# Optimization experiments

Hardware: AMD Instinct MI355X
Metric: run time of the kernel (lower is better)

The kernel has to match this reference:

```python
import jax, jax.numpy as jnp
import numpy as np

NQ = 4      # n_qubits
T = 512     # seq_lenght
H = 1024    # hidden_size
F = 64      # input feature size
B = 16      # batch size (hardcoded in original module)


def _circuit_tables(nq):
    idx = np.arange(2 ** nq)
    # BasicEntanglerLayers CNOT ring: (0,1),(1,2),...,(n-1,0) for n>2; single CNOT for n==2
    pairs = [(i, (i + 1) % nq) for i in range(nq)] if nq > 2 else [(0, 1)]
    perms = []
    for c, t in pairs:  # CNOT as a basis-state permutation (qubit 0 = MSB)
        ctrl = (idx >> (nq - 1 - c)) & 1
        perms.append(idx ^ (ctrl << (nq - 1 - t)))
    bits = (idx[:, None] >> (nq - 1 - np.arange(nq))[None, :]) & 1
    signs = (1.0 - 2.0 * bits).astype(np.float32)  # (2**nq, nq), <Z_q> signs
    return perms, signs

_PERMS, _SIGNS = _circuit_tables(NQ)
_SIGNS_J = jnp.asarray(_SIGNS)


def circuit_expvals(theta):
    """theta: (..., NQ) total RX angle per wire (AngleEmbedding RX + entangler RX).
    Returns (..., NQ) PauliZ expvals after product-RX state + CNOT ring."""
    half = 0.5 * theta
    a0 = jnp.cos(half).astype(jnp.complex64)
    a1 = (-1j * jnp.sin(half)).astype(jnp.complex64)
    state = jnp.ones(theta.shape[:-1] + (1,), dtype=jnp.complex64)
    for q in range(NQ):  # build product state, qubit 0 most significant
        amp = jnp.stack([a0[..., q], a1[..., q]], axis=-1)
        state = (state[..., :, None] * amp[..., None, :]).reshape(theta.shape[:-1] + (-1,))
    for perm in _PERMS:  # CNOT ring = permutations of the computational basis
        state = state[..., perm]
    probs = state.real ** 2 + state.imag ** 2  # (..., 2**NQ)
    return probs @ _SIGNS_J                     # (..., NQ)


def qlstm_last(x, w4, Wy, by, Wf, bf, Wi, bi, Wu, bu, Wo, bo):
    """x: (B, T, feat). Dense params are stacked per-timestep along axis 0 (T,...)
    (the original creates a fresh nn.Dense every loop iteration).
    Returns the hidden state at the last timestep, (B, H)."""
    h0 = jnp.zeros((x.shape[0], H), dtype=x.dtype)
    c0 = jnp.zeros((x.shape[0], H), dtype=x.dtype)

    def step(carry, inp):
        h, c = carry
        x_t, wy, byt, wf, bft, wi, bit_, wu, but, wo, bot = inp
        v = jnp.concatenate([h, x_t], axis=1)
        y = v @ wy + byt                                   # (B, NQ)
        z = circuit_expvals(y[None] + w4[:, None, :])      # (4, B, NQ), shared input, 4 gate weights
        f = jax.nn.sigmoid(z[0]) @ wf + bft                # NOTE: no activation after Dense, as in source
        i = jax.nn.sigmoid(z[1]) @ wi + bit_
        g = jnp.tanh(z[2]) @ wu + but
        o = jax.nn.sigmoid(z[3]) @ wo + bot
        c = f * c + i * g
        h = o * jnp.tanh(c)
        return (h, c), None

    xs = (jnp.swapaxes(x, 0, 1), Wy, by, Wf, bf, Wi, bi, Wu, bu, Wo, bo)
    (h, _), _ = jax.lax.scan(step, (h0, c0), xs)
    return h


def setup_inputs() -> dict:
    key = jax.random.key(0)
    ks = jax.random.split(key, 16)
    def w(k, shape, fan_in):
        return jax.random.normal(k, shape, jnp.float32) / np.sqrt(fan_in)
    inp = {"x": jax.random.normal(ks[0], (B, T, F), jnp.float32)}
    # quantum weights (n_qlayers=1, n_qubits) per gate
    for n, k in zip(["qwf", "qwi", "qwu", "qwo"], jax.random.split(ks[1], 4)):
        inp[n] = jax.random.uniform(k, (1, NQ), jnp.float32, -1.0, 1.0)
    # encoder: per-timestep Dense stacks
    inp["Wy_e"] = w(ks[2], (T, H + F, NQ), H + F); inp["by_e"] = jnp.zeros((T, NQ), jnp.float32)
    for n, k in zip(["f", "i", "u", "o"], jax.random.split(ks[3], 4)):
        inp["W" + n + "_e"] = w(k, (T, NQ, H), NQ)
        inp["b" + n + "_e"] = jnp.zeros((T, H), jnp.float32)
    # decoder: input feature size 1
    inp["Wy_d"] = w(ks[4], (T, H + 1, NQ), H + 1); inp["by_d"] = jnp.zeros((T, NQ), jnp.float32)
    for n, k in zip(["f", "i", "u", "o"], jax.random.split(ks[5], 4)):
        inp["W" + n + "_d"] = w(k, (T, NQ, H), NQ)
        inp["b" + n + "_d"] = jnp.zeros((T, H), jnp.float32)
    # final Dense(seq_lenght)
    inp["Wt"] = w(ks[6], (H, T), H); inp["bt"] = jnp.zeros((T,), jnp.float32)
    return inp


def reference(x, qwf, qwi, qwu, qwo,
              Wy_e, by_e, Wf_e, bf_e, Wi_e, bi_e, Wu_e, bu_e, Wo_e, bo_e,
              Wy_d, by_d, Wf_d, bf_d, Wi_d, bi_d, Wu_d, bu_d, Wo_d, bo_d,
              Wt, bt):
    w4 = jnp.stack([qwf[0], qwi[0], qwu[0], qwo[0]])  # only layer-0 row is used by the qnode
    h_enc = qlstm_last(x, w4, Wy_e, by_e, Wf_e, bf_e, Wi_e, bi_e, Wu_e, bu_e, Wo_e, bo_e)
    x2 = h_enc[:, :, None]                 # (B, H, 1)
    h_dec = qlstm_last(x2[:, :T, :], w4, Wy_d, by_d, Wf_d, bf_d, Wi_d, bi_d, Wu_d, bu_d, Wo_d, bo_d)
    target = h_dec @ Wt + bt               # (B, T)
    return target[:, :, None]              # (B, T, 1)
```

## Files before the change

kernel.cpp:

```cpp
#include <hip/hip_runtime.h>

#define Tn 512
#define Hn 1024
#define Fn 64
#define NTH 512
#define NW (NTH / 64)

#define STEPB (6u * 512u * 16u)
#define MAXTOFF (511u * STEPB)
#define REC_PASS ((unsigned long long)Tn * STEPB)
#define YXE_OFF (2ull * REC_PASS)
#define WS_NEED (2ull * REC_PASS + 16ull * 512ull * 16ull)

typedef unsigned u32x4 __attribute__((ext_vector_type(4)));
typedef __fp16 h2 __attribute__((ext_vector_type(2)));

struct QParams {
  const float *x;
  const float *qw0, *qw1, *qw2, *qw3;
  const float *Wy_e, *by_e, *Wf_e, *bf_e, *Wi_e, *bi_e, *Wu_e, *bu_e, *Wo_e, *bo_e;
  const float *Wy_d, *by_d, *Wf_d, *bf_d, *Wi_d, *bi_d, *Wu_d, *bu_d, *Wo_d, *bo_d;
  const float *Wt, *bt;
  float *out;
};

#define BAR()                                                                  \
  do {                                                                         \
    asm volatile("s_waitcnt lgkmcnt(0)" ::: "memory");                         \
    __builtin_amdgcn_s_barrier();                                              \
    asm volatile("" ::: "memory");                                             \
  } while (0)
#define WAIT_VM(N)                                                             \
  do {                                                                         \
    asm volatile("s_waitcnt vmcnt(" #N ")" ::: "memory");                      \
    __builtin_amdgcn_sched_barrier(0);                                         \
  } while (0)

template <int CTRL, int RM, int BM, bool BC>
__device__ __forceinline__ float dppadd(float x) {
  int t = __builtin_amdgcn_update_dpp(0, __builtin_bit_cast(int, x), CTRL, RM,
                                      BM, BC);
  return x + __builtin_bit_cast(float, t);
}
template <int CTRL>
__device__ __forceinline__ float dppmov(float x) {
  int t = __builtin_amdgcn_update_dpp(0, __builtin_bit_cast(int, x), CTRL, 0xF,
                                      0xF, true);
  return __builtin_bit_cast(float, t);
}
__device__ __forceinline__ float wave_sum63(float x) {
  x = dppadd<0xB1, 0xF, 0xF, true>(x);
  x = dppadd<0x4E, 0xF, 0xF, true>(x);
  x = dppadd<0x141, 0xF, 0xF, true>(x);
  x = dppadd<0x140, 0xF, 0xF, true>(x);
  x = dppadd<0x142, 0xA, 0xF, false>(x);
  x = dppadd<0x143, 0xC, 0xF, false>(x);
  return x;
}
__device__ __forceinline__ float tanhc(float c) {
  float e = __builtin_amdgcn_exp2f(c * 2.885390081777927f);
  return fmaf(-2.f, __builtin_amdgcn_rcpf(e + 1.f), 1.f);
}
__device__ __forceinline__ h2 pk2(float a, float b) {
  return __builtin_amdgcn_cvt_pkrtz(a, b);
}
__device__ __forceinline__ h2 uh(unsigned u) { return __builtin_bit_cast(h2, u); }
__device__ __forceinline__ float fdot2f(h2 a, h2 b, float c) {
#if __has_builtin(__builtin_amdgcn_fdot2)
  return __builtin_amdgcn_fdot2(a, b, c, false);
#else
  float d;
  asm("v_dot2_f32_f16 %0, %1, %2, %3" : "=v"(d) : "v"(a), "v"(b), "v"(c));
  return d;
#endif
}
__device__ __forceinline__ unsigned pkh(float a, float b) {
  h2 h;
  h.x = (__fp16)a;
  h.y = (__fp16)b;
  return __builtin_bit_cast(unsigned, h);
}

struct LaneCtx {
  int tid, lane, wid;
  unsigned jt16;
  bool q1, q2;
  float w4lane;
  float mlane, alane, klane;
};
struct SBase {
  unsigned long long a[6];
};

__global__ __launch_bounds__(512) void qprep_kernel(QParams p, char *ws) {
  int t = blockIdx.x;
  const bool dec = (t >= 512);
  if (dec) t -= 512;
  const int j = threadIdx.x;

  const float *Wg0 = dec ? p.Wf_d : p.Wf_e, *Wg1 = dec ? p.Wi_d : p.Wi_e;
  const float *Wg2 = dec ? p.Wu_d : p.Wu_e, *Wg3 = dec ? p.Wo_d : p.Wo_e;
  const float *bf = dec ? p.bf_d : p.bf_e, *bi = dec ? p.bi_d : p.bi_e;
  const float *bu = dec ? p.bu_d : p.bu_e, *bo = dec ? p.bo_d : p.bo_e;
  const float *Wy = dec ? p.Wy_d : p.Wy_e;
  const int K = dec ? (Hn + 1) : (Hn + Fn);

  u32x4 *dst = (u32x4 *)(ws + (dec ? REC_PASS : 0));
  const int rbase = t * 6 * 512 + j;
  const int t4 = t * 4096;
  const float *Wg[4] = {Wg0, Wg1, Wg2, Wg3};
#pragma unroll
  for (int g = 0; g < 4; ++g) {
    u32x4 v;
    v.x = pkh(Wg[g][t4 + 0 * 1024 + j], Wg[g][t4 + 1 * 1024 + j]);
    v.y = pkh(Wg[g][t4 + 2 * 1024 + j], Wg[g][t4 + 3 * 1024 + j]);
    v.z = pkh(Wg[g][t4 + 0 * 1024 + j + 512], Wg[g][t4 + 1 * 1024 + j + 512]);
    v.w = pkh(Wg[g][t4 + 2 * 1024 + j + 512], Wg[g][t4 + 3 * 1024 + j + 512]);
    dst[rbase + g * 512] = v;
  }
  {
    const int tb = t * 1024;
    u32x4 v = {pkh(bf[tb + j], bf[tb + j + 512]),
               pkh(bi[tb + j], bi[tb + j + 512]),
               pkh(bu[tb + j], bu[tb + j + 512]),
               pkh(bo[tb + j], bo[tb + j + 512])};
    dst[rbase + 4 * 512] = v;
  }
  {
    const float4 w0 = *(const float4 *)(Wy + ((size_t)t * K + j) * 4);
    const float4 w1 = *(const float4 *)(Wy + ((size_t)t * K + j + 512) * 4);
    u32x4 v = {pkh(w0.x, w1.x), pkh(w0.y, w1.y), pkh(w0.z, w1.z),
               pkh(w0.w, w1.w)};
    dst[rbase + 5 * 512] = v;
  }

  if (!dec && j < 16) {
    const int b = j;
    float a0 = p.by_e[t * 4 + 0], a1 = p.by_e[t * 4 + 1],
          a2 = p.by_e[t * 4 + 2], a3 = p.by_e[t * 4 + 3];
#pragma unroll 8
    for (int k = 0; k < 64; ++k) {
      const float xv = p.x[((size_t)b * Tn + t) * Fn + k];
      const float4 wr =
          *(const float4 *)(p.Wy_e + ((size_t)t * (Hn + Fn) + Hn + k) * 4);
      a0 = fmaf(xv, wr.x, a0);
      a1 = fmaf(xv, wr.y, a1);
      a2 = fmaf(xv, wr.z, a2);
      a3 = fmaf(xv, wr.w, a3);
    }
    ((float4 *)(ws + YXE_OFF))[(size_t)b * Tn + t] =
        make_float4(a0, a1, a2, a3);
  }
}

struct Regs {
  u32x4 c0, c1, c2, c3, c4, c5;
};

__device__ __forceinline__ void issue_pf(Regs &r, const SBase &sb,
                                         unsigned voff) {
  asm volatile("global_load_dwordx4 %0, %1, %2" : "=v"(r.c5) : "v"(voff), "s"(sb.a[5]));
  asm volatile("global_load_dwordx4 %0, %1, %2" : "=v"(r.c0) : "v"(voff), "s"(sb.a[0]));
  asm volatile("global_load_dwordx4 %0, %1, %2" : "=v"(r.c1) : "v"(voff), "s"(sb.a[1]));
  asm volatile("global_load_dwordx4 %0, %1, %2" : "=v"(r.c2) : "v"(voff), "s"(sb.a[2]));
  asm volatile("global_load_dwordx4 %0, %1, %2" : "=v"(r.c3) : "v"(voff), "s"(sb.a[3]));
  asm volatile("global_load_dwordx4 %0, %1, %2" : "=v"(r.c4) : "v"(voff), "s"(sb.a[4]));
}

template <int PAR>
__device__ __forceinline__ void
qstep(int t, Regs &r, unsigned &toff, const SBase &sb, const LaneCtx &L,
      float *red_t, const float *yxby_l, float &h0, float &h1, float &c0,
      float &c1, h2 &hp) {
  const float yxs = yxby_l[t * 4 + (L.lane & 3)];
  WAIT_VM(18);
  float a0 = fdot2f(hp, uh(r.c5.x), 0.f);
  float a1 = fdot2f(hp, uh(r.c5.y), 0.f);
  float a2 = fdot2f(hp, uh(r.c5.z), 0.f);
  float a3 = fdot2f(hp, uh(r.c5.w), 0.f);
  a0 = wave_sum63(a0);
  a1 = wave_sum63(a1);
  a2 = wave_sum63(a2);
  a3 = wave_sum63(a3);
  if (L.lane == 63) {
    red_t[PAR * 32 + 0 * 8 + L.wid] = a0;
    red_t[PAR * 32 + 1 * 8 + L.wid] = a1;
    red_t[PAR * 32 + 2 * 8 + L.wid] = a2;
    red_t[PAR * 32 + 3 * 8 + L.wid] = a3;
  }
  BAR();
  const float4 rA = *(const float4 *)&red_t[PAR * 32 + (L.lane & 3) * 8 + 0];
  const float4 rB = *(const float4 *)&red_t[PAR * 32 + (L.lane & 3) * 8 + 4];
  const float yq =
      ((rA.x + rA.y) + (rA.z + rA.w)) + ((rB.x + rB.y) + (rB.z + rB.w));
  const float ang = yq + yxs + L.w4lane;
  const float cc = __cosf(ang);
  const float t1 = dppmov<0xB1>(cc);
  const float d1 = cc * t1;
  const float t2 = dppmov<0x4E>(d1);
  const float d2 = d1 * t2;
  const float zu = t1 * t2;
  const float zv = cc * t2;
  const float z = L.q2 ? (L.q1 ? d2 : zv) : (L.q1 ? d1 : zu);
  const float s =
      __builtin_amdgcn_rcpf(1.f + __builtin_amdgcn_exp2f(L.klane * z));
  const float act = fmaf(s, L.mlane, L.alane);
  const float actn = dppmov<0xB1>(act);
  const unsigned apk = __builtin_bit_cast(unsigned, pk2(act, actn));
  const h2 F01 = uh((unsigned)__builtin_amdgcn_readlane(apk, 0));
  const h2 F23 = uh((unsigned)__builtin_amdgcn_readlane(apk, 2));
  const h2 I01 = uh((unsigned)__builtin_amdgcn_readlane(apk, 4));
  const h2 I23 = uh((unsigned)__builtin_amdgcn_readlane(apk, 6));
  const h2 U01 = uh((unsigned)__builtin_amdgcn_readlane(apk, 8));
  const h2 U23 = uh((unsigned)__builtin_amdgcn_readlane(apk, 10));
  const h2 O01 = uh((unsigned)__builtin_amdgcn_readlane(apk, 12));
  const h2 O23 = uh((unsigned)__builtin_amdgcn_readlane(apk, 14));
  const h2 bgf = uh(r.c4.x), bgi = uh(r.c4.y), bgu = uh(r.c4.z),
           bgo = uh(r.c4.w);
  const float fv0 = fdot2f(F01, uh(r.c0.x), fdot2f(F23, uh(r.c0.y), (float)bgf.x));
  const float fv1 = fdot2f(F01, uh(r.c0.z), fdot2f(F23, uh(r.c0.w), (float)bgf.y));
  const float iv0 = fdot2f(I01, uh(r.c1.x), fdot2f(I23, uh(r.c1.y), (float)bgi.x));
  const float iv1 = fdot2f(I01, uh(r.c1.z), fdot2f(I23, uh(r.c1.w), (float)bgi.y));
  const float uv0 = fdot2f(U01, uh(r.c2.x), fdot2f(U23, uh(r.c2.y), (float)bgu.x));
  const float uv1 = fdot2f(U01, uh(r.c2.z), fdot2f(U23, uh(r.c2.w), (float)bgu.y));
  const float ov0 = fdot2f(O01, uh(r.c3.x), fdot2f(O23, uh(r.c3.y), (float)bgo.x));
  const float ov1 = fdot2f(O01, uh(r.c3.z), fdot2f(O23, uh(r.c3.w), (float)bgo.y));
  c0 = fmaf(fv0, c0, iv0 * uv0);
  h0 = ov0 * tanhc(c0);
  c1 = fmaf(fv1, c1, iv1 * uv1);
  h1 = ov1 * tanhc(c1);
  hp = pk2(h0, h1);
  issue_pf(r, sb, L.jt16 + toff);
  toff = toff + STEPB;
  if (toff > MAXTOFF) toff = MAXTOFF;
}

__device__ __forceinline__ void run_pass(const SBase &sb, const LaneCtx &L,
                                         float *red_t, const float *yxby_l,
                                         float &h0, float &h1, float &c0,
                                         float &c1) {
  Regs R0, R1, R2, R3;
  issue_pf(R0, sb, L.jt16 + 0 * STEPB);
  issue_pf(R1, sb, L.jt16 + 1 * STEPB);
  issue_pf(R2, sb, L.jt16 + 2 * STEPB);
  issue_pf(R3, sb, L.jt16 + 3 * STEPB);
  unsigned toff = 4 * STEPB;
  h2 hp = pk2(0.f, 0.f);
  for (int t = 0; t < Tn; t += 4) {
    qstep<0>(t + 0, R0, toff, sb, L, red_t, yxby_l, h0, h1, c0, c1, hp);
    qstep<1>(t + 1, R1, toff, sb, L, red_t, yxby_l, h0, h1, c0, c1, hp);
    qstep<0>(t + 2, R2, toff, sb, L, red_t, yxby_l, h0, h1, c0, c1, hp);
    qstep<1>(t + 3, R3, toff, sb, L, red_t, yxby_l, h0, h1, c0, c1, hp);
  }
  asm volatile("s_waitcnt vmcnt(0)" ::: "memory");
  __builtin_amdgcn_sched_barrier(0);
}

__global__ __launch_bounds__(NTH, 2) void qlstm_f16_kernel(QParams p,
                                                           char *ws) {
  const int b = blockIdx.x;
  LaneCtx L;
  L.tid = threadIdx.x;
  L.lane = L.tid & 63;
  L.wid = L.tid >> 6;
  L.jt16 = (unsigned)L.tid * 16u;
  const int q = L.lane & 3, g = (L.lane >> 2) & 3;
  L.q1 = q & 1;
  L.q2 = q & 2;
  {
    const float *qwp =
        (g == 0) ? p.qw0 : (g == 1) ? p.qw1 : (g == 2) ? p.qw2 : p.qw3;
    L.w4lane = qwp[q];
  }
  L.mlane = (g == 2) ? 2.f : 1.f;
  L.alane = 1.f - L.mlane;
  L.klane = -L.mlane * 1.4426950408889634f;

  __shared__ __align__(16) float red_t[2 * 4 * 8];
  __shared__ __align__(16) float yxby_l[Tn * 4];
  __shared__ __align__(16) float hbuf[Hn];

  SBase sbE, sbD;
#pragma unroll
  for (int k = 0; k < 6; ++k) {
    sbE.a[k] = (unsigned long long)ws + (unsigned long long)k * 8192ull;
    sbD.a[k] = (unsigned long long)ws + REC_PASS + (unsigned long long)k * 8192ull;
  }

  ((float4 *)yxby_l)[L.tid] =
      ((const float4 *)(ws + YXE_OFF))[(size_t)b * Tn + L.tid];
  float h0 = 0.f, h1 = 0.f, c0 = 0.f, c1 = 0.f;
  __syncthreads();

  run_pass(sbE, L, red_t, yxby_l, h0, h1, c0, c1);

  __syncthreads();
  hbuf[L.tid] = h0;
  hbuf[L.tid + NTH] = h1;
  __syncthreads();
  {
    const float hv = hbuf[L.tid];
    const float4 wx =
        *(const float4 *)(p.Wy_d + ((size_t)L.tid * (Hn + 1) + Hn) * 4);
    const float4 bd = *(const float4 *)(p.by_d + L.tid * 4);
    ((float4 *)yxby_l)[L.tid] =
        make_float4(fmaf(hv, wx.x, bd.x), fmaf(hv, wx.y, bd.y),
                    fmaf(hv, wx.z, bd.z), fmaf(hv, wx.w, bd.w));
  }
  h0 = h1 = c0 = c1 = 0.f;
  __syncthreads();

  run_pass(sbD, L, red_t, yxby_l, h0, h1, c0, c1);

  __syncthreads();
  hbuf[L.tid] = h0;
  hbuf[L.tid + NTH] = h1;
  __syncthreads();
  {
    float acc = p.bt[L.tid];
    const float4 *h4 = (const float4 *)hbuf;
#pragma unroll 4
    for (int j4 = 0; j4 < Hn / 4; ++j4) {
      const float4 hv = h4[j4];
      acc = fmaf(hv.x, p.Wt[(j4 * 4 + 0) * Tn + L.tid], acc);
      acc = fmaf(hv.y, p.Wt[(j4 * 4 + 1) * Tn + L.tid], acc);
      acc = fmaf(hv.z, p.Wt[(j4 * 4 + 2) * Tn + L.tid], acc);
      acc = fmaf(hv.w, p.Wt[(j4 * 4 + 3) * Tn + L.tid], acc);
    }
    p.out[(size_t)b * Tn + L.tid] = acc;
  }
}

__device__ __forceinline__ float sum8_all(float x) {
  x = dppadd<0xB1, 0xF, 0xF, true>(x);
  x = dppadd<0x4E, 0xF, 0xF, true>(x);
  x = dppadd<0x141, 0xF, 0xF, true>(x);
  return x;
}

struct WB {
  float w[32];
  float bb[8];
  float4 wy0, wy1;
  float4 wyx;
  float xv;
};

template <bool DEC>
__device__ __forceinline__ WB
pf_fb(int t, int b, int tid, const float *__restrict__ x,
      const float *__restrict__ Wy, const float *__restrict__ Wf,
      const float *__restrict__ bfp, const float *__restrict__ Wi,
      const float *__restrict__ bip, const float *__restrict__ Wu,
      const float *__restrict__ bup, const float *__restrict__ Wo,
      const float *__restrict__ bop) {
  WB d;
  const int K = DEC ? (Hn + 1) : (Hn + Fn);
  const int g0 = t * 4096 + tid;
#pragma unroll
  for (int e = 0; e < 2; ++e) {
    const int ge = g0 + e * 512;
#pragma unroll
    for (int n = 0; n < 4; ++n) {
      d.w[e * 16 + 0 * 4 + n] = Wf[ge + n * 1024];
      d.w[e * 16 + 1 * 4 + n] = Wi[ge + n * 1024];
      d.w[e * 16 + 2 * 4 + n] = Wu[ge + n * 1024];
      d.w[e * 16 + 3 * 4 + n] = Wo[ge + n * 1024];
    }
    const int be = t * 1024 + tid + e * 512;
    d.bb[e * 4 + 0] = bfp[be];
    d.bb[e * 4 + 1] = bip[be];
    d.bb[e * 4 + 2] = bup[be];
    d.bb[e * 4 + 3] = bop[be];
  }
  d.wy0 = *(const float4 *)(Wy + (t * K + tid) * 4);
  d.wy1 = *(const float4 *)(Wy + (t * K + tid + 512) * 4);
  if (!DEC) {
    if (tid < Fn) {
      d.wyx = *(const float4 *)(Wy + (t * K + Hn + tid) * 4);
      d.xv = x[(b * Tn + t) * Fn + tid];
    }
  } else {
    if (tid == 0) d.wyx = *(const float4 *)(Wy + (t * K + Hn) * 4);
  }
  return d;
}

template <bool DEC, int PAR>
__device__ __forceinline__ void
step_fb(int t, int tn, const WB &rd, WB &wr, int b, const LaneCtx &L,
        const float *__restrict__ x, const float *__restrict__ Wy,
        const float *__restrict__ Wf, const float *__restrict__ bfp,
        const float *__restrict__ Wi, const float *__restrict__ bip,
        const float *__restrict__ Wu, const float *__restrict__ bup,
        const float *__restrict__ Wo, const float *__restrict__ bop,
        float4 (*red4)[NW], const float *by_l, const float *henc_s, float &h0,
        float &h1, float &c0, float &c1) {
  float a0 = h0 * rd.wy0.x, a1 = h0 * rd.wy0.y, a2 = h0 * rd.wy0.z,
        a3 = h0 * rd.wy0.w;
  a0 = fmaf(h1, rd.wy1.x, a0);
  a1 = fmaf(h1, rd.wy1.y, a1);
  a2 = fmaf(h1, rd.wy1.z, a2);
  a3 = fmaf(h1, rd.wy1.w, a3);
  if (!DEC) {
    if (L.tid < Fn) {
      a0 = fmaf(rd.xv, rd.wyx.x, a0);
      a1 = fmaf(rd.xv, rd.wyx.y, a1);
      a2 = fmaf(rd.xv, rd.wyx.z, a2);
      a3 = fmaf(rd.xv, rd.wyx.w, a3);
    }
  } else {
    if (L.tid == 0) {
      const float xv = henc_s[t];
      a0 = fmaf(xv, rd.wyx.x, a0);
      a1 = fmaf(xv, rd.wyx.y, a1);
      a2 = fmaf(xv, rd.wyx.z, a2);
      a3 = fmaf(xv, rd.wyx.w, a3);
    }
  }
  a0 = wave_sum63(a0);
  a1 = wave_sum63(a1);
  a2 = wave_sum63(a2);
  a3 = wave_sum63(a3);
  if (L.lane == 63) red4[PAR][L.wid] = make_float4(a0, a1, a2, a3);
  wr = pf_fb<DEC>(tn, b, L.tid, x, Wy, Wf, bfp, Wi, bip, Wu, bup, Wo, bop);
  BAR();
  float4 rv = red4[PAR][L.lane & 7];
  const float byq = by_l[t * 4 + (L.lane & 3)];
  float y0 = sum8_all(rv.x), y1 = sum8_all(rv.y), y2 = sum8_all(rv.z),
        y3 = sum8_all(rv.w);
  const float yq = L.q2 ? (L.q1 ? y3 : y2) : (L.q1 ? y1 : y0);
  const float ang = yq + byq + L.w4lane;
  const float cc = __cosf(ang);
  const float t1 = dppmov<0xB1>(cc);
  const float d1 = cc * t1;
  const float t2 = dppmov<0x4E>(d1);
  const float d2 = d1 * t2;
  const float zu = t1 * t2;
  const float zv = cc * t2;
  const float z = L.q2 ? (L.q1 ? d2 : zv) : (L.q1 ? d1 : zu);
  const float s =
      __builtin_amdgcn_rcpf(1.f + __builtin_amdgcn_exp2f(L.klane * z));
  const float act = fmaf(s, L.mlane, L.alane);
#define RL(n)                                                                  \
  __builtin_bit_cast(float,                                                    \
                     __builtin_amdgcn_readlane(__builtin_bit_cast(int, act), n))
  const float f0 = RL(0), f1 = RL(1), f2 = RL(2), f3 = RL(3);
  const float i0 = RL(4), i1 = RL(5), i2 = RL(6), i3 = RL(7);
  const float u0 = RL(8), u1 = RL(9), u2 = RL(10), u3 = RL(11);
  const float o0 = RL(12), o1 = RL(13), o2 = RL(14), o3 = RL(15);
#undef RL
#pragma unroll
  for (int e = 0; e < 2; ++e) {
    float fv = rd.bb[e * 4 + 0], iv = rd.bb[e * 4 + 1], uv = rd.bb[e * 4 + 2],
          ov = rd.bb[e * 4 + 3];
    fv = fmaf(f0, rd.w[e * 16 + 0], fv);
    fv = fmaf(f1, rd.w[e * 16 + 1], fv);
    fv = fmaf(f2, rd.w[e * 16 + 2], fv);
    fv = fmaf(f3, rd.w[e * 16 + 3], fv);
    iv = fmaf(i0, rd.w[e * 16 + 4], iv);
    iv = fmaf(i1, rd.w[e * 16 + 5], iv);
    iv = fmaf(i2, rd.w[e * 16 + 6], iv);
    iv = fmaf(i3, rd.w[e * 16 + 7], iv);
    uv = fmaf(u0, rd.w[e * 16 + 8], uv);
    uv = fmaf(u1, rd.w[e * 16 + 9], uv);
    uv = fmaf(u2, rd.w[e * 16 + 10], uv);
    uv = fmaf(u3, rd.w[e * 16 + 11], uv);
    ov = fmaf(o0, rd.w[e * 16 + 12], ov);
    ov = fmaf(o1, rd.w[e * 16 + 13], ov);
    ov = fmaf(o2, rd.w[e * 16 + 14], ov);
    ov = fmaf(o3, rd.w[e * 16 + 15], ov);
    float &cr = e ? c1 : c0;
    float &hr = e ? h1 : h0;
    const float cn = fmaf(fv, cr, iv * uv);
    cr = cn;
    hr = ov * tanhc(cn);
  }
}

template <bool DEC>
__device__ void lstm_pass_fb(int b, const LaneCtx &L,
                             const float *__restrict__ x,
                             const float *__restrict__ Wy,
                             const float *__restrict__ by,
                             const float *__restrict__ Wf,
                             const float *__restrict__ bfp,
                             const float *__restrict__ Wi,
                             const float *__restrict__ bip,
                             const float *__restrict__ Wu,
                             const float *__restrict__ bup,
                             const float *__restrict__ Wo,
                             const float *__restrict__ bop,
                             float4 (*red4)[NW], float *by_l,
                             const float *henc_s, float &h0, float &h1,
                             float &c0, float &c1) {
#pragma unroll
  for (int i = 0; i < (Tn * 4) / NTH; ++i)
    by_l[L.tid + i * NTH] = by[L.tid + i * NTH];
  __syncthreads();
  WB bufA = pf_fb<DEC>(0, b, L.tid, x, Wy, Wf, bfp, Wi, bip, Wu, bup, Wo, bop);
  WB bufB;
  for (int t = 0; t < Tn; t += 2) {
    step_fb<DEC, 0>(t, t + 1, bufA, bufB, b, L, x, Wy, Wf, bfp, Wi, bip, Wu,
                    bup, Wo, bop, red4, by_l, henc_s, h0, h1, c0, c1);
    step_fb<DEC, 1>(t + 1, (t + 2 < Tn) ? (t + 2) : (Tn - 1), bufB, bufA, b, L,
                    x, Wy, Wf, bfp, Wi, bip, Wu, bup, Wo, bop, red4, by_l,
                    henc_s, h0, h1, c0, c1);
  }
}

__global__ __launch_bounds__(NTH, 2) void qlstm_fb_kernel(QParams p) {
  const int b = blockIdx.x;
  LaneCtx L;
  L.tid = threadIdx.x;
  L.lane = L.tid & 63;
  L.wid = L.tid >> 6;
  L.jt16 = (unsigned)L.tid * 16u;
  const int q = L.lane & 3, g = (L.lane >> 2) & 3;
  L.q1 = q & 1;
  L.q2 = q & 2;
  {
    const float *qwp =
        (g == 0) ? p.qw0 : (g == 1) ? p.qw1 : (g == 2) ? p.qw2 : p.qw3;
    L.w4lane = qwp[q];
  }
  L.mlane = (g == 2) ? 2.f : 1.f;
  L.alane = 1.f - L.mlane;
  L.klane = -L.mlane * 1.4426950408889634f;

  __shared__ float4 red4[2][NW];
  __shared__ float by_l[Tn * 4];
  __shared__ float henc_s[Hn];
  __shared__ float hst[Hn];

  float h0 = 0.f, h1 = 0.f, c0 = 0.f, c1 = 0.f;

  lstm_pass_fb<false>(b, L, p.x, p.Wy_e, p.by_e, p.Wf_e, p.bf_e, p.Wi_e,
                      p.bi_e, p.Wu_e, p.bu_e, p.Wo_e, p.bo_e, red4, by_l,
                      henc_s, h0, h1, c0, c1);
  henc_s[L.tid] = h0;
  henc_s[L.tid + NTH] = h1;
  h0 = h1 = c0 = c1 = 0.f;
  __syncthreads();
  lstm_pass_fb<true>(b, L, nullptr, p.Wy_d, p.by_d, p.Wf_d, p.bf_d, p.Wi_d,
                     p.bi_d, p.Wu_d, p.bu_d, p.Wo_d, p.bo_d, red4, by_l,
                     henc_s, h0, h1, c0, c1);
  hst[L.tid] = h0;
  hst[L.tid + NTH] = h1;
  __syncthreads();
  {
    float acc = p.bt[L.tid];
    const float4 *h4 = (const float4 *)hst;
#pragma unroll 4
    for (int j4 = 0; j4 < Hn / 4; ++j4) {
      const float4 hv = h4[j4];
      acc = fmaf(hv.x, p.Wt[(j4 * 4 + 0) * Tn + L.tid], acc);
      acc = fmaf(hv.y, p.Wt[(j4 * 4 + 1) * Tn + L.tid], acc);
      acc = fmaf(hv.z, p.Wt[(j4 * 4 + 2) * Tn + L.tid], acc);
      acc = fmaf(hv.w, p.Wt[(j4 * 4 + 3) * Tn + L.tid], acc);
    }
    p.out[(size_t)b * Tn + L.tid] = acc;
  }
}

extern "C" void kernel_launch(void *const *d_in, const int *in_sizes, int n_in,
                              void *d_out, int out_size, void *d_ws,
                              size_t ws_size, hipStream_t stream) {
  QParams p;
  p.x = (const float *)d_in[0];
  p.qw0 = (const float *)d_in[1];
  p.qw1 = (const float *)d_in[2];
  p.qw2 = (const float *)d_in[3];
  p.qw3 = (const float *)d_in[4];
  p.Wy_e = (const float *)d_in[5];
  p.by_e = (const float *)d_in[6];
  p.Wf_e = (const float *)d_in[7];
  p.bf_e = (const float *)d_in[8];
  p.Wi_e = (const float *)d_in[9];
  p.bi_e = (const float *)d_in[10];
  p.Wu_e = (const float *)d_in[11];
  p.bu_e = (const float *)d_in[12];
  p.Wo_e = (const float *)d_in[13];
  p.bo_e = (const float *)d_in[14];
  p.Wy_d = (const float *)d_in[15];
  p.by_d = (const float *)d_in[16];
  p.Wf_d = (const float *)d_in[17];
  p.bf_d = (const float *)d_in[18];
  p.Wi_d = (const float *)d_in[19];
  p.bi_d = (const float *)d_in[20];
  p.Wu_d = (const float *)d_in[21];
  p.bu_d = (const float *)d_in[22];
  p.Wo_d = (const float *)d_in[23];
  p.bo_d = (const float *)d_in[24];
  p.Wt = (const float *)d_in[25];
  p.bt = (const float *)d_in[26];
  p.out = (float *)d_out;

  if (ws_size >= WS_NEED) {
    char *ws = (char *)d_ws;
    hipLaunchKernelGGL(qprep_kernel, dim3(1024), dim3(512), 0, stream, p, ws);
    hipLaunchKernelGGL(qlstm_f16_kernel, dim3(16), dim3(NTH), 0, stream, p,
                       ws);
  } else {
    hipLaunchKernelGGL(qlstm_fb_kernel, dim3(16), dim3(NTH), 0, stream, p);
  }
}
```

Measured before the change: 691.0 us.

## Halve recurrent-kernel block to 256 threads with four hidden units per thread

The fp16 recurrent kernel now runs 256 threads per batch block, and each thread owns four hidden units instead of two. The prep kernel repacks the weights into a 12-stream layout to match, and the per-step prefetch issues 12 loads. Fewer waves shrink the cross-wave reduction and barrier cost of each serial timestep. In exchange, each thread does twice the arithmetic, holds more registers for four in-flight prefetch buffers, and the memory latency per step is spread across fewer waves.

```diff
diff --git a/kernel.cpp b/kernel.cpp
--- a/kernel.cpp
+++ b/kernel.cpp
@@ -3,10 +3,10 @@
 #define Tn 512
 #define Hn 1024
 #define Fn 64
-#define NTH 512
+#define NTH 256
 #define NW (NTH / 64)
 
-#define STEPB (6u * 512u * 16u)
+#define STEPB (12u * 256u * 16u)
 #define MAXTOFF (511u * STEPB)
 #define REC_PASS ((unsigned long long)Tn * STEPB)
 #define YXE_OFF (2ull * REC_PASS)
@@ -89,10 +89,10 @@
   float mlane, alane, klane;
 };
 struct SBase {
-  unsigned long long a[6];
+  unsigned long long a[12];
 };
 
-__global__ __launch_bounds__(512) void qprep_kernel(QParams p, char *ws) {
+__global__ __launch_bounds__(256) void qprep_kernel(QParams p, char *ws) {
   int t = blockIdx.x;
   const bool dec = (t >= 512);
   if (dec) t -= 512;
@@ -105,33 +105,42 @@
   const float *Wy = dec ? p.Wy_d : p.Wy_e;
   const int K = dec ? (Hn + 1) : (Hn + Fn);
 
-  u32x4 *dst = (u32x4 *)(ws + (dec ? REC_PASS : 0));
-  const int rbase = t * 6 * 512 + j;
+  char *base = ws + (dec ? REC_PASS : 0) + (size_t)t * STEPB;
   const int t4 = t * 4096;
   const float *Wg[4] = {Wg0, Wg1, Wg2, Wg3};
 #pragma unroll
   for (int g = 0; g < 4; ++g) {
-    u32x4 v;
-    v.x = pkh(Wg[g][t4 + 0 * 1024 + j], Wg[g][t4 + 1 * 1024 + j]);
-    v.y = pkh(Wg[g][t4 + 2 * 1024 + j], Wg[g][t4 + 3 * 1024 + j]);
-    v.z = pkh(Wg[g][t4 + 0 * 1024 + j + 512], Wg[g][t4 + 1 * 1024 + j + 512]);
-    v.w = pkh(Wg[g][t4 + 2 * 1024 + j + 512], Wg[g][t4 + 3 * 1024 + j + 512]);
-    dst[rbase + g * 512] = v;
+#pragma unroll
+    for (int k = 0; k < 2; ++k) {
+      const int jb = j + 512 * k;
+      u32x4 v;
+      v.x = pkh(Wg[g][t4 + 0 * 1024 + jb], Wg[g][t4 + 1 * 1024 + jb]);
+      v.y = pkh(Wg[g][t4 + 2 * 1024 + jb], Wg[g][t4 + 3 * 1024 + jb]);
+      v.z = pkh(Wg[g][t4 + 0 * 1024 + jb + 256], Wg[g][t4 + 1 * 1024 + jb + 256]);
+      v.w = pkh(Wg[g][t4 + 2 * 1024 + jb + 256], Wg[g][t4 + 3 * 1024 + jb + 256]);
+      *(u32x4 *)(base + (g * 2 + k) * 4096 + j * 16) = v;
+    }
   }
   {
     const int tb = t * 1024;
-    u32x4 v = {pkh(bf[tb + j], bf[tb + j + 512]),
-               pkh(bi[tb + j], bi[tb + j + 512]),
-               pkh(bu[tb + j], bu[tb + j + 512]),
-               pkh(bo[tb + j], bo[tb + j + 512])};
-    dst[rbase + 4 * 512] = v;
+#pragma unroll
+    for (int k = 0; k < 2; ++k) {
+      const int jb = tb + j + 512 * k;
+      u32x4 v = {pkh(bf[jb], bf[jb + 256]), pkh(bi[jb], bi[jb + 256]),
+                 pkh(bu[jb], bu[jb + 256]), pkh(bo[jb], bo[jb + 256])};
+      *(u32x4 *)(base + (8 + k) * 4096 + j * 16) = v;
+    }
   }
   {
-    const float4 w0 = *(const float4 *)(Wy + ((size_t)t * K + j) * 4);
-    const float4 w1 = *(const float4 *)(Wy + ((size_t)t * K + j + 512) * 4);
-    u32x4 v = {pkh(w0.x, w1.x), pkh(w0.y, w1.y), pkh(w0.z, w1.z),
-               pkh(w0.w, w1.w)};
-    dst[rbase + 5 * 512] = v;
+#pragma unroll
+    for (int k = 0; k < 2; ++k) {
+      const int jb = j + 512 * k;
+      const float4 w0 = *(const float4 *)(Wy + ((size_t)t * K + jb) * 4);
+      const float4 w1 = *(const float4 *)(Wy + ((size_t)t * K + jb + 256) * 4);
+      u32x4 v = {pkh(w0.x, w1.x), pkh(w0.y, w1.y), pkh(w0.z, w1.z),
+                 pkh(w0.w, w1.w)};
+      *(u32x4 *)(base + (10 + k) * 4096 + j * 16) = v;
+    }
   }
 
   if (!dec && j < 16) {
@@ -154,45 +163,56 @@
 }
 
 struct Regs {
-  u32x4 c0, c1, c2, c3, c4, c5;
+  u32x4 g0, g1, g2, g3, g4, g5, g6, g7;
+  u32x4 b8, b9;
+  u32x4 w10, w11;
 };
 
 __device__ __forceinline__ void issue_pf(Regs &r, const SBase &sb,
                                          unsigned voff) {
-  asm volatile("global_load_dwordx4 %0, %1, %2" : "=v"(r.c5) : "v"(voff), "s"(sb.a[5]));
-  asm volatile("global_load_dwordx4 %0, %1, %2" : "=v"(r.c0) : "v"(voff), "s"(sb.a[0]));
-  asm volatile("global_load_dwordx4 %0, %1, %2" : "=v"(r.c1) : "v"(voff), "s"(sb.a[1]));
-  asm volatile("global_load_dwordx4 %0, %1, %2" : "=v"(r.c2) : "v"(voff), "s"(sb.a[2]));
-  asm volatile("global_load_dwordx4 %0, %1, %2" : "=v"(r.c3) : "v"(voff), "s"(sb.a[3]));
-  asm volatile("global_load_dwordx4 %0, %1, %2" : "=v"(r.c4) : "v"(voff), "s"(sb.a[4]));
+  asm volatile("global_load_dwordx4 %0, %1, %2" : "=v"(r.w10) : "v"(voff), "s"(sb.a[10]));
+  asm volatile("global_load_dwordx4 %0, %1, %2" : "=v"(r.w11) : "v"(voff), "s"(sb.a[11]));
+  asm volatile("global_load_dwordx4 %0, %1, %2" : "=v"(r.g0) : "v"(voff), "s"(sb.a[0]));
+  asm volatile("global_load_dwordx4 %0, %1, %2" : "=v"(r.g1) : "v"(voff), "s"(sb.a[1]));
+  asm volatile("global_load_dwordx4 %0, %1, %2" : "=v"(r.g2) : "v"(voff), "s"(sb.a[2]));
+  asm volatile("global_load_dwordx4 %0, %1, %2" : "=v"(r.g3) : "v"(voff), "s"(sb.a[3]));
+  asm volatile("global_load_dwordx4 %0, %1, %2" : "=v"(r.g4) : "v"(voff), "s"(sb.a[4]));
+  asm volatile("global_load_dwordx4 %0, %1, %2" : "=v"(r.g5) : "v"(voff), "s"(sb.a[5]));
+  asm volatile("global_load_dwordx4 %0, %1, %2" : "=v"(r.g6) : "v"(voff), "s"(sb.a[6]));
+  asm volatile("global_load_dwordx4 %0, %1, %2" : "=v"(r.g7) : "v"(voff), "s"(sb.a[7]));
+  asm volatile("global_load_dwordx4 %0, %1, %2" : "=v"(r.b8) : "v"(voff), "s"(sb.a[8]));
+  asm volatile("global_load_dwordx4 %0, %1, %2" : "=v"(r.b9) : "v"(voff), "s"(sb.a[9]));
 }
 
 template <int PAR>
 __device__ __forceinline__ void
 qstep(int t, Regs &r, unsigned &toff, const SBase &sb, const LaneCtx &L,
-      float *red_t, const float *yxby_l, float &h0, float &h1, float &c0,
-      float &c1, h2 &hp) {
+      float *red_t, const float *yxby_l, float &h0, float &h1, float &h2r,
+      float &h3, float &c0, float &c1, float &c2r, float &c3, h2 &hp0,
+      h2 &hp1) {
   const float yxs = yxby_l[t * 4 + (L.lane & 3)];
-  WAIT_VM(18);
-  float a0 = fdot2f(hp, uh(r.c5.x), 0.f);
-  float a1 = fdot2f(hp, uh(r.c5.y), 0.f);
-  float a2 = fdot2f(hp, uh(r.c5.z), 0.f);
-  float a3 = fdot2f(hp, uh(r.c5.w), 0.f);
+  WAIT_VM(36);
+  float a0 = fdot2f(hp0, uh(r.w10.x), 0.f);
+  float a1 = fdot2f(hp0, uh(r.w10.y), 0.f);
+  float a2 = fdot2f(hp0, uh(r.w10.z), 0.f);
+  float a3 = fdot2f(hp0, uh(r.w10.w), 0.f);
+  a0 = fdot2f(hp1, uh(r.w11.x), a0);
+  a1 = fdot2f(hp1, uh(r.w11.y), a1);
+  a2 = fdot2f(hp1, uh(r.w11.z), a2);
+  a3 = fdot2f(hp1, uh(r.w11.w), a3);
   a0 = wave_sum63(a0);
   a1 = wave_sum63(a1);
   a2 = wave_sum63(a2);
   a3 = wave_sum63(a3);
   if (L.lane == 63) {
-    red_t[PAR * 32 + 0 * 8 + L.wid] = a0;
-    red_t[PAR * 32 + 1 * 8 + L.wid] = a1;
-    red_t[PAR * 32 + 2 * 8 + L.wid] = a2;
-    red_t[PAR * 32 + 3 * 8 + L.wid] = a3;
+    red_t[PAR * 16 + 0 * 4 + L.wid] = a0;
+    red_t[PAR * 16 + 1 * 4 + L.wid] = a1;
+    red_t[PAR * 16 + 2 * 4 + L.wid] = a2;
+    red_t[PAR * 16 + 3 * 4 + L.wid] = a3;
   }
   BAR();
-  const float4 rA = *(const float4 *)&red_t[PAR * 32 + (L.lane & 3) * 8 + 0];
-  const float4 rB = *(const float4 *)&red_t[PAR * 32 + (L.lane & 3) * 8 + 4];
-  const float yq =
-      ((rA.x + rA.y) + (rA.z + rA.w)) + ((rB.x + rB.y) + (rB.z + rB.w));
+  const float4 rA = *(const float4 *)&red_t[PAR * 16 + (L.lane & 3) * 4];
+  const float yq = (rA.x + rA.y) + (rA.z + rA.w);
   const float ang = yq + yxs + L.w4lane;
   const float cc = __cosf(ang);
   const float t1 = dppmov<0xB1>(cc);
@@ -215,21 +235,36 @@
   const h2 U23 = uh((unsigned)__builtin_amdgcn_readlane(apk, 10));
   const h2 O01 = uh((unsigned)__builtin_amdgcn_readlane(apk, 12));
   const h2 O23 = uh((unsigned)__builtin_amdgcn_readlane(apk, 14));
-  const h2 bgf = uh(r.c4.x), bgi = uh(r.c4.y), bgu = uh(r.c4.z),
-           bgo = uh(r.c4.w);
-  const float fv0 = fdot2f(F01, uh(r.c0.x), fdot2f(F23, uh(r.c0.y), (float)bgf.x));
-  const float fv1 = fdot2f(F01, uh(r.c0.z), fdot2f(F23, uh(r.c0.w), (float)bgf.y));
-  const float iv0 = fdot2f(I01, uh(r.c1.x), fdot2f(I23, uh(r.c1.y), (float)bgi.x));
-  const float iv1 = fdot2f(I01, uh(r.c1.z), fdot2f(I23, uh(r.c1.w), (float)bgi.y));
-  const float uv0 = fdot2f(U01, uh(r.c2.x), fdot2f(U23, uh(r.c2.y), (float)bgu.x));
-  const float uv1 = fdot2f(U01, uh(r.c2.z), fdot2f(U23, uh(r.c2.w), (float)bgu.y));
-  const float ov0 = fdot2f(O01, uh(r.c3.x), fdot2f(O23, uh(r.c3.y), (float)bgo.x));
-  const float ov1 = fdot2f(O01, uh(r.c3.z), fdot2f(O23, uh(r.c3.w), (float)bgo.y));
+  const h2 bF01 = uh(r.b8.x), bI01 = uh(r.b8.y), bU01 = uh(r.b8.z),
+           bO01 = uh(r.b8.w);
+  const h2 bF23 = uh(r.b9.x), bI23 = uh(r.b9.y), bU23 = uh(r.b9.z),
+           bO23 = uh(r.b9.w);
+  const float fv0 = fdot2f(F01, uh(r.g0.x), fdot2f(F23, uh(r.g0.y), (float)bF01.x));
+  const float fv1 = fdot2f(F01, uh(r.g0.z), fdot2f(F23, uh(r.g0.w), (float)bF01.y));
+  const float fv2 = fdot2f(F01, uh(r.g1.x), fdot2f(F23, uh(r.g1.y), (float)bF23.x));
+  const float fv3 = fdot2f(F01, uh(r.g1.z), fdot2f(F23, uh(r.g1.w), (float)bF23.y));
+  const float iv0 = fdot2f(I01, uh(r.g2.x), fdot2f(I23, uh(r.g2.y), (float)bI01.x));
+  const float iv1 = fdot2f(I01, uh(r.g2.z), fdot2f(I23, uh(r.g2.w), (float)bI01.y));
+  const float iv2 = fdot2f(I01, uh(r.g3.x), fdot2f(I23, uh(r.g3.y), (float)bI23.x));
+  const float iv3 = fdot2f(I01, uh(r.g3.z), fdot2f(I23, uh(r.g3.w), (float)bI23.y));
+  const float uv0 = fdot2f(U01, uh(r.g4.x), fdot2f(U23, uh(r.g4.y), (float)bU01.x));
+  const float uv1 = fdot2f(U01, uh(r.g4.z), fdot2f(U23, uh(r.g4.w), (float)bU01.y));
+  const float uv2 = fdot2f(U01, uh(r.g5.x), fdot2f(U23, uh(r.g5.y), (float)bU23.x));
+  const float uv3 = fdot2f(U01, uh(r.g5.z), fdot2f(U23, uh(r.g5.w), (float)bU23.y));
+  const float ov0 = fdot2f(O01, uh(r.g6.x), fdot2f(O23, uh(r.g6.y), (float)bO01.x));
+  const float ov1 = fdot2f(O01, uh(r.g6.z), fdot2f(O23, uh(r.g6.w), (float)bO01.y));
+  const float ov2 = fdot2f(O01, uh(r.g7.x), fdot2f(O23, uh(r.g7.y), (float)bO23.x));
+  const float ov3 = fdot2f(O01, uh(r.g7.z), fdot2f(O23, uh(r.g7.w), (float)bO23.y));
   c0 = fmaf(fv0, c0, iv0 * uv0);
   h0 = ov0 * tanhc(c0);
   c1 = fmaf(fv1, c1, iv1 * uv1);
   h1 = ov1 * tanhc(c1);
-  hp = pk2(h0, h1);
+  c2r = fmaf(fv2, c2r, iv2 * uv2);
+  h2r = ov2 * tanhc(c2r);
+  c3 = fmaf(fv3, c3, iv3 * uv3);
+  h3 = ov3 * tanhc(c3);
+  hp0 = pk2(h0, h1);
+  hp1 = pk2(h2r, h3);
   issue_pf(r, sb, L.jt16 + toff);
   toff = toff + STEPB;
   if (toff > MAXTOFF) toff = MAXTOFF;
@@ -237,26 +272,28 @@
 
 __device__ __forceinline__ void run_pass(const SBase &sb, const LaneCtx &L,
                                          float *red_t, const float *yxby_l,
-                                         float &h0, float &h1, float &c0,
-                                         float &c1) {
+                                         float &h0, float &h1, float &h2r,
+                                         float &h3, float &c0, float &c1,
+                                         float &c2r, float &c3) {
   Regs R0, R1, R2, R3;
+  WAIT_VM(0);
   issue_pf(R0, sb, L.jt16 + 0 * STEPB);
   issue_pf(R1, sb, L.jt16 + 1 * STEPB);
   issue_pf(R2, sb, L.jt16 + 2 * STEPB);
   issue_pf(R3, sb, L.jt16 + 3 * STEPB);
   unsigned toff = 4 * STEPB;
-  h2 hp = pk2(0.f, 0.f);
+  h2 hp0 = pk2(0.f, 0.f), hp1 = pk2(0.f, 0.f);
   for (int t = 0; t < Tn; t += 4) {
-    qstep<0>(t + 0, R0, toff, sb, L, red_t, yxby_l, h0, h1, c0, c1, hp);
-    qstep<1>(t + 1, R1, toff, sb, L, red_t, yxby_l, h0, h1, c0, c1, hp);
-    qstep<0>(t + 2, R2, toff, sb, L, red_t, yxby_l, h0, h1, c0, c1, hp);
-    qstep<1>(t + 3, R3, toff, sb, L, red_t, yxby_l, h0, h1, c0, c1, hp);
+    qstep<0>(t + 0, R0, toff, sb, L, red_t, yxby_l, h0, h1, h2r, h3, c0, c1, c2r, c3, hp0, hp1);
+    qstep<1>(t + 1, R1, toff, sb, L, red_t, yxby_l, h0, h1, h2r, h3, c0, c1, c2r, c3, hp0, hp1);
+    qstep<0>(t + 2, R2, toff, sb, L, red_t, yxby_l, h0, h1, h2r, h3, c0, c1, c2r, c3, hp0, hp1);
+    qstep<1>(t + 3, R3, toff, sb, L, red_t, yxby_l, h0, h1, h2r, h3, c0, c1, c2r, c3, hp0, hp1);
   }
   asm volatile("s_waitcnt vmcnt(0)" ::: "memory");
   __builtin_amdgcn_sched_barrier(0);
 }
 
-__global__ __launch_bounds__(NTH, 2) void qlstm_f16_kernel(QParams p,
+__global__ __launch_bounds__(NTH, 1) void qlstm_f16_kernel(QParams p,
                                                            char *ws) {
   const int b = blockIdx.x;
   LaneCtx L;
@@ -276,61 +313,75 @@
   L.alane = 1.f - L.mlane;
   L.klane = -L.mlane * 1.4426950408889634f;
 
-  __shared__ __align__(16) float red_t[2 * 4 * 8];
+  __shared__ __align__(16) float red_t[2 * 4 * NW];
   __shared__ __align__(16) float yxby_l[Tn * 4];
   __shared__ __align__(16) float hbuf[Hn];
 
   SBase sbE, sbD;
 #pragma unroll
-  for (int k = 0; k < 6; ++k) {
-    sbE.a[k] = (unsigned long long)ws + (unsigned long long)k * 8192ull;
-    sbD.a[k] = (unsigned long long)ws + REC_PASS + (unsigned long long)k * 8192ull;
-  }
-
-  ((float4 *)yxby_l)[L.tid] =
-      ((const float4 *)(ws + YXE_OFF))[(size_t)b * Tn + L.tid];
-  float h0 = 0.f, h1 = 0.f, c0 = 0.f, c1 = 0.f;
-  __syncthreads();
-
-  run_pass(sbE, L, red_t, yxby_l, h0, h1, c0, c1);
+  for (int k = 0; k < 12; ++k) {
+    sbE.a[k] = (unsigned long long)ws + (unsigned long long)k * 4096ull;
+    sbD.a[k] = (unsigned long long)ws + REC_PASS + (unsigned long long)k * 4096ull;
+  }
+
+#pragma unroll
+  for (int i = 0; i < 2; ++i)
+    ((float4 *)yxby_l)[L.tid + i * NTH] =
+        ((const float4 *)(ws + YXE_OFF))[(size_t)b * Tn + L.tid + i * NTH];
+  float h0 = 0.f, h1 = 0.f, h2r = 0.f, h3 = 0.f;
+  float c0 = 0.f, c1 = 0.f, c2r = 0.f, c3 = 0.f;
+  __syncthreads();
+
+  run_pass(sbE, L, red_t, yxby_l, h0, h1, h2r, h3, c0, c1, c2r, c3);
 
   __syncthreads();
   hbuf[L.tid] = h0;
-  hbuf[L.tid + NTH] = h1;
-  __syncthreads();
-  {
-    const float hv = hbuf[L.tid];
+  hbuf[L.tid + 256] = h1;
+  hbuf[L.tid + 512] = h2r;
+  hbuf[L.tid + 768] = h3;
+  __syncthreads();
+#pragma unroll
+  for (int i = 0; i < 2; ++i) {
+    const int t2 = L.tid + i * NTH;
+    const float hv = hbuf[t2];
     const float4 wx =
-        *(const float4 *)(p.Wy_d + ((size_t)L.tid * (Hn + 1) + Hn) * 4);
-    const float4 bd = *(const float4 *)(p.by_d + L.tid * 4);
-    ((float4 *)yxby_l)[L.tid] =
+        *(const float4 *)(p.Wy_d + ((size_t)t2 * (Hn + 1) + Hn) * 4);
+    const float4 bd = *(const float4 *)(p.by_d + t2 * 4);
+    ((float4 *)yxby_l)[t2] =
         make_float4(fmaf(hv, wx.x, bd.x), fmaf(hv, wx.y, bd.y),
                     fmaf(hv, wx.z, bd.z), fmaf(hv, wx.w, bd.w));
   }
-  h0 = h1 = c0 = c1 = 0.f;
-  __syncthreads();
-
-  run_pass(sbD, L, red_t, yxby_l, h0, h1, c0, c1);
+  h0 = h1 = h2r = h3 = 0.f;
+  c0 = c1 = c2r = c3 = 0.f;
+  __syncthreads();
+
+  run_pass(sbD, L, red_t, yxby_l, h0, h1, h2r, h3, c0, c1, c2r, c3);
 
   __syncthreads();
   hbuf[L.tid] = h0;
-  hbuf[L.tid + NTH] = h1;
-  __syncthreads();
-  {
-    float acc = p.bt[L.tid];
+  hbuf[L.tid + 256] = h1;
+  hbuf[L.tid + 512] = h2r;
+  hbuf[L.tid + 768] = h3;
+  __syncthreads();
+#pragma unroll
+  for (int i = 0; i < 2; ++i) {
+    const int t2 = L.tid + i * NTH;
+    float acc = p.bt[t2];
     const float4 *h4 = (const float4 *)hbuf;
 #pragma unroll 4
     for (int j4 = 0; j4 < Hn / 4; ++j4) {
       const float4 hv = h4[j4];
-      acc = fmaf(hv.x, p.Wt[(j4 * 4 + 0) * Tn + L.tid], acc);
-      acc = fmaf(hv.y, p.Wt[(j4 * 4 + 1) * Tn + L.tid], acc);
-      acc = fmaf(hv.z, p.Wt[(j4 * 4 + 2) * Tn + L.tid], acc);
-      acc = fmaf(hv.w, p.Wt[(j4 * 4 + 3) * Tn + L.tid], acc);
-    }
-    p.out[(size_t)b * Tn + L.tid] = acc;
-  }
-}
-
+      acc = fmaf(hv.x, p.Wt[(j4 * 4 + 0) * Tn + t2], acc);
+      acc = fmaf(hv.y, p.Wt[(j4 * 4 + 1) * Tn + t2], acc);
+      acc = fmaf(hv.z, p.Wt[(j4 * 4 + 2) * Tn + t2], acc);
+      acc = fmaf(hv.w, p.Wt[(j4 * 4 + 3) * Tn + t2], acc);
+    }
+    p.out[(size_t)b * Tn + t2] = acc;
+  }
+}
+
+#define FNTH 512
+#define FNW (FNTH / 64)
 __device__ __forceinline__ float sum8_all(float x) {
   x = dppadd<0xB1, 0xF, 0xF, true>(x);
   x = dppadd<0x4E, 0xF, 0xF, true>(x);
@@ -386,15 +437,21 @@
   return d;
 }
 
+struct FLane {
+  int tid, lane, wid;
+  bool q1, q2;
+  float w4lane, mlane, alane, klane;
+};
+
 template <bool DEC, int PAR>
 __device__ __forceinline__ void
-step_fb(int t, int tn, const WB &rd, WB &wr, int b, const LaneCtx &L,
+step_fb(int t, int tn, const WB &rd, WB &wr, int b, const FLane &L,
         const float *__restrict__ x, const float *__restrict__ Wy,
         const float *__restrict__ Wf, const float *__restrict__ bfp,
         const float *__restrict__ Wi, const float *__restrict__ bip,
         const float *__restrict__ Wu, const float *__restrict__ bup,
         const float *__restrict__ Wo, const float *__restrict__ bop,
-        float4 (*red4)[NW], const float *by_l, const float *henc_s, float &h0,
+        float4 (*red4)[FNW], const float *by_l, const float *henc_s, float &h0,
         float &h1, float &c0, float &c1) {
   float a0 = h0 * rd.wy0.x, a1 = h0 * rd.wy0.y, a2 = h0 * rd.wy0.z,
         a3 = h0 * rd.wy0.w;
@@ -479,7 +536,7 @@
 }
 
 template <bool DEC>
-__device__ void lstm_pass_fb(int b, const LaneCtx &L,
+__device__ void lstm_pass_fb(int b, const FLane &L,
                              const float *__restrict__ x,
                              const float *__restrict__ Wy,
                              const float *__restrict__ by,
@@ -491,12 +548,12 @@
                              const float *__restrict__ bup,
                              const float *__restrict__ Wo,
                              const float *__restrict__ bop,
-                             float4 (*red4)[NW], float *by_l,
+                             float4 (*red4)[FNW], float *by_l,
                              const float *henc_s, float &h0, float &h1,
                              float &c0, float &c1) {
 #pragma unroll
-  for (int i = 0; i < (Tn * 4) / NTH; ++i)
-    by_l[L.tid + i * NTH] = by[L.tid + i * NTH];
+  for (int i = 0; i < (Tn * 4) / FNTH; ++i)
+    by_l[L.tid + i * FNTH] = by[L.tid + i * FNTH];
   __syncthreads();
   WB bufA = pf_fb<DEC>(0, b, L.tid, x, Wy, Wf, bfp, Wi, bip, Wu, bup, Wo, bop);
   WB bufB;
@@ -509,13 +566,12 @@
   }
 }
 
-__global__ __launch_bounds__(NTH, 2) void qlstm_fb_kernel(QParams p) {
+__global__ __launch_bounds__(FNTH, 2) void qlstm_fb_kernel(QParams p) {
   const int b = blockIdx.x;
-  LaneCtx L;
+  FLane L;
   L.tid = threadIdx.x;
   L.lane = L.tid & 63;
   L.wid = L.tid >> 6;
-  L.jt16 = (unsigned)L.tid * 16u;
   const int q = L.lane & 3, g = (L.lane >> 2) & 3;
   L.q1 = q & 1;
   L.q2 = q & 2;
@@ -528,7 +584,7 @@
   L.alane = 1.f - L.mlane;
   L.klane = -L.mlane * 1.4426950408889634f;
 
-  __shared__ float4 red4[2][NW];
+  __shared__ float4 red4[2][FNW];
   __shared__ float by_l[Tn * 4];
   __shared__ float henc_s[Hn];
   __shared__ float hst[Hn];
@@ -539,14 +595,14 @@
                       p.bi_e, p.Wu_e, p.bu_e, p.Wo_e, p.bo_e, red4, by_l,
                       henc_s, h0, h1, c0, c1);
   henc_s[L.tid] = h0;
-  henc_s[L.tid + NTH] = h1;
+  henc_s[L.tid + FNTH] = h1;
   h0 = h1 = c0 = c1 = 0.f;
   __syncthreads();
   lstm_pass_fb<true>(b, L, nullptr, p.Wy_d, p.by_d, p.Wf_d, p.bf_d, p.Wi_d,
                      p.bi_d, p.Wu_d, p.bu_d, p.Wo_d, p.bo_d, red4, by_l,
                      henc_s, h0, h1, c0, c1);
   hst[L.tid] = h0;
-  hst[L.tid + NTH] = h1;
+  hst[L.tid + FNTH] = h1;
   __syncthreads();
   {
     float acc = p.bt[L.tid];
@@ -598,10 +654,10 @@
 
   if (ws_size >= WS_NEED) {
     char *ws = (char *)d_ws;
-    hipLaunchKernelGGL(qprep_kernel, dim3(1024), dim3(512), 0, stream, p, ws);
+    hipLaunchKernelGGL(qprep_kernel, dim3(1024), dim3(256), 0, stream, p, ws);
     hipLaunchKernelGGL(qlstm_f16_kernel, dim3(16), dim3(NTH), 0, stream, p,
                        ws);
   } else {
-    hipLaunchKernelGGL(qlstm_fb_kernel, dim3(16), dim3(NTH), 0, stream, p);
-  }
-}
+    hipLaunchKernelGGL(qlstm_fb_kernel, dim3(16), dim3(FNTH), 0, stream, p);
+  }
+}
```

Result: slower. 786.8 us (+13.9%).
